# Kernel optimization log

Hardware: AMD Instinct MI355X
Metric: run time of the kernel (lower is better)

## Reference

```python
import jax, jax.numpy as jnp
import numpy as np

L, H, P = 16384, 1024, 512  # seq len, model width, state size (conj_sym: P = ssm_size//2)
DT_MIN, DT_MAX = 1e-3, 1e-1
STEP_RESCALE = 1.0


def setup_inputs() -> dict:
    key = jax.random.key(0)
    ks = jax.random.split(key, 7)
    input_sequence = jax.random.normal(ks[0], (L, H), dtype=jnp.float32)
    # Lambda: stable diagonal (Re < 0), like DPLR-HiPPO (Re = -0.5, spread imag parts)
    Lambda_re = -0.5 - jax.random.uniform(ks[1], (P,), dtype=jnp.float32)
    Lambda_im = 10.0 * jax.random.normal(ks[2], (P,), dtype=jnp.float32)
    # B (P,H,2) and C (H,P,2): real/imag stacked parameterization
    B = jax.random.normal(ks[3], (P, H, 2), dtype=jnp.float32) / np.float32(np.sqrt(H))
    C = jax.random.normal(ks[4], (H, P, 2), dtype=jnp.float32) / np.float32(np.sqrt(P))
    D = jax.random.normal(ks[5], (H,), dtype=jnp.float32)
    log_step = (jax.random.uniform(ks[6], (P, 1), dtype=jnp.float32)
                * (np.log(DT_MAX) - np.log(DT_MIN)) + np.log(DT_MIN)).astype(jnp.float32)
    return {"input_sequence": input_sequence, "Lambda_re": Lambda_re,
            "Lambda_im": Lambda_im, "B": B, "C": C, "D": D, "log_step": log_step}


def _binop(q_i, q_j):
    # diagonal linear recurrence composition; elementwise, so works on stacked arrays
    A_i, b_i = q_i
    A_j, b_j = q_j
    return (A_j * A_i, A_j * b_i + b_j)


def reference(input_sequence, Lambda_re, Lambda_im, B, C, D, log_step):
    Lambda = Lambda_re + 1j * Lambda_im                      # (P,) complex64
    B_tilde = B[..., 0] + 1j * B[..., 1]                     # (P,H)
    C_tilde = C[..., 0] + 1j * C[..., 1]                     # (H,P)
    Delta = STEP_RESCALE * jnp.exp(log_step[:, 0])           # (P,)
    # ZOH discretization
    Lambda_bar = jnp.exp(Lambda * Delta)                     # (P,)
    B_bar = ((Lambda_bar - 1.0) / Lambda)[:, None] * B_tilde # (P,H)
    # per-step scan elements
    Lambda_elements = jnp.broadcast_to(Lambda_bar, (input_sequence.shape[0], P))
    Bu_elements = jnp.einsum('lh,ph->lp', input_sequence, B_bar)  # (L,P) complex
    _, xs = jax.lax.associative_scan(_binop, (Lambda_elements, Bu_elements))
    # conj_sym readout: 2 * Re(C x)
    ys = 2.0 * jnp.einsum('lp,hp->lh', xs, C_tilde).real     # (L,H) float32
    return ys + input_sequence * D
```

## Files before the change

### kernel.cpp

```cpp
#include <hip/hip_runtime.h>
#include <math.h>

#define LL 16384
#define HH 1024
#define PP 512
#define NP2 1024
#define CHUNK 64
#define NCHUNK 256
#define BM 128
#define BN 128
#define BK 32

typedef unsigned short u16;
typedef __attribute__((ext_vector_type(8))) short bf16x8;
typedef __attribute__((ext_vector_type(4))) float f32x4;

__device__ __forceinline__ u16 f2bf(float f) {
    unsigned u = __float_as_uint(f);
    unsigned r = 0x7fffu + ((u >> 16) & 1u);
    return (u16)((u + r) >> 16);
}
__device__ __forceinline__ float bf2f(u16 x) {
    return __uint_as_float(((unsigned)x) << 16);
}

__device__ __forceinline__ void gload_lds16(const void* g, void* l) {
    __builtin_amdgcn_global_load_lds(
        (const __attribute__((address_space(1))) unsigned int*)g,
        (__attribute__((address_space(3))) unsigned int*)l, 16, 0, 0);
}

__global__ void k_setup(const float* __restrict__ lre, const float* __restrict__ lim,
                        const float* __restrict__ logstep,
                        float* __restrict__ gre, float* __restrict__ gim,
                        float* __restrict__ lbre, float* __restrict__ lbim,
                        float* __restrict__ ltre, float* __restrict__ ltim) {
    int p = threadIdx.x;
    if (p >= PP) return;
    float dt = expf(logstep[p]);
    float ar = lre[p], ai = lim[p];
    float e = expf(ar * dt);
    float s, c;
    sincosf(ai * dt, &s, &c);
    float Lr = e * c, Li = e * s;
    lbre[p] = Lr; lbim[p] = Li;
    float nr = Lr - 1.0f, ni = Li;
    float den = ar * ar + ai * ai;
    gre[p] = (nr * ar + ni * ai) / den;
    gim[p] = (ni * ar - nr * ai) / den;
    float tr = Lr, ti = Li;
    for (int i = 0; i < 6; i++) {
        float rr = tr * tr - ti * ti;
        float mm = 2.0f * tr * ti;
        tr = rr; ti = mm;
    }
    ltre[p] = tr; ltim[p] = ti;
}

__global__ void k_bbar(const float* __restrict__ B,
                       const float* __restrict__ gre, const float* __restrict__ gim,
                       u16* __restrict__ bb) {
    int t = blockIdx.x * 256 + threadIdx.x;
    int p = t >> 10;
    float2 b = ((const float2*)B)[t];
    float gr = gre[p], gi = gim[p];
    bb[t] = f2bf(gr * b.x - gi * b.y);
    bb[(size_t)PP * HH + t] = f2bf(gr * b.y + gi * b.x);
}

__global__ void k_cprep(const float* __restrict__ C, u16* __restrict__ cp) {
    int t = blockIdx.x * 256 + threadIdx.x;
    int h = t >> 9, p = t & 511;
    float2 c = ((const float2*)C)[t];
    cp[(size_t)h * NP2 + p] = f2bf(c.x);
    cp[(size_t)h * NP2 + PP + p] = f2bf(-c.y);
}

__global__ void k_cvt(const float* __restrict__ s, u16* __restrict__ d) {
    size_t i = ((size_t)blockIdx.x * 256 + threadIdx.x) * 4;
    float4 v = *(const float4*)&s[i];
    unsigned lo = (unsigned)f2bf(v.x) | ((unsigned)f2bf(v.y) << 16);
    unsigned hi = (unsigned)f2bf(v.z) | ((unsigned)f2bf(v.w) << 16);
    *(uint2*)&d[i] = make_uint2(lo, hi);
}

template<int FUSE>
__global__ __launch_bounds__(256) void k_gemm(
        const u16* __restrict__ A, const u16* __restrict__ Bt,
        void* __restrict__ outp, const int K,
        const u16* __restrict__ ubf, const float* __restrict__ Din) {
    __shared__ u16 lA[BM * BK];
    __shared__ u16 lB[BN * BK];
    const int b = blockIdx.x;
    const int xcd = b & 7, s = b >> 3;
    const int m0 = (xcd * 16 + (s >> 3)) * BM;
    const int n0 = (s & 7) * BN;
    const int N = 8 * BN;
    const int t = threadIdx.x;
    const int lane = t & 63, wid = t >> 6;
    const int wm = (wid >> 1) * 64, wn = (wid & 1) * 64;
    const int frow = lane & 15, quad = lane >> 4;

    f32x4 acc[4][4];
    #pragma unroll
    for (int i = 0; i < 4; i++)
        #pragma unroll
        for (int j = 0; j < 4; j++) acc[i][j] = (f32x4){0.f, 0.f, 0.f, 0.f};

    const int sr = t >> 2, sc = (t & 3) * 8;
    const u16* gA = A + (size_t)(m0 + sr) * K + sc;
    const u16* gB = Bt + (size_t)(n0 + sr) * K + sc;
    u16* dA = &lA[sr * BK + sc];
    u16* dB = &lB[sr * BK + sc];

    for (int k0 = 0; k0 < K; k0 += BK) {
        __syncthreads();
        gload_lds16(gA + k0, dA);
        gload_lds16(gA + (size_t)64 * K + k0, dA + 64 * BK);
        gload_lds16(gB + k0, dB);
        gload_lds16(gB + (size_t)64 * K + k0, dB + 64 * BK);
        __syncthreads();
        bf16x8 av[4], bv[4];
        #pragma unroll
        for (int i = 0; i < 4; i++)
            av[i] = *(const bf16x8*)&lA[(wm + i * 16 + frow) * BK + quad * 8];
        #pragma unroll
        for (int j = 0; j < 4; j++)
            bv[j] = *(const bf16x8*)&lB[(wn + j * 16 + frow) * BK + quad * 8];
        #pragma unroll
        for (int i = 0; i < 4; i++)
            #pragma unroll
            for (int j = 0; j < 4; j++)
                acc[i][j] = __builtin_amdgcn_mfma_f32_16x16x32_bf16(
                    av[i], bv[j], acc[i][j], 0, 0, 0);
    }

    #pragma unroll
    for (int i = 0; i < 4; i++) {
        const int row = m0 + wm + i * 16 + quad * 4;
        #pragma unroll
        for (int j = 0; j < 4; j++) {
            const int col = n0 + wn + j * 16 + frow;
            f32x4 v = acc[i][j];
            if (FUSE) {
                float* Cout = (float*)outp;
                const float dv = Din[col];
                #pragma unroll
                for (int r = 0; r < 4; r++) {
                    const size_t o = (size_t)(row + r) * N + col;
                    Cout[o] = 2.0f * v[r] + bf2f(ubf[o]) * dv;
                }
            } else {
                u16* Cb = (u16*)outp;
                #pragma unroll
                for (int r = 0; r < 4; r++)
                    Cb[(size_t)(row + r) * N + col] = f2bf(v[r]);
            }
        }
    }
}

__global__ void k_scan1(const u16* __restrict__ bu,
                        const float* __restrict__ lbre, const float* __restrict__ lbim,
                        float* __restrict__ fr, float* __restrict__ fi) {
    int p = blockIdx.x * 256 + threadIdx.x;
    int c = blockIdx.y;
    float ar = lbre[p], ai = lbim[p];
    float xr = 0.f, xi = 0.f;
    const u16* b = bu + (size_t)c * CHUNK * NP2 + p;
    for (int j = 0; j < CHUNK; j++) {
        float br = bf2f(b[0]), bi = bf2f(b[PP]);
        float nr = ar * xr - ai * xi + br;
        float ni = ar * xi + ai * xr + bi;
        xr = nr; xi = ni;
        b += NP2;
    }
    fr[c * PP + p] = xr;
    fi[c * PP + p] = xi;
}

__global__ __launch_bounds__(256) void k_scan2(
        const float* __restrict__ fr, const float* __restrict__ fi,
        const float* __restrict__ ltre, const float* __restrict__ ltim,
        float* __restrict__ cr, float* __restrict__ ci) {
    __shared__ float Ar[NCHUNK], Ai[NCHUNK], br[NCHUNK], bi[NCHUNK];
    const int p = blockIdx.x;
    const int c = threadIdx.x;
    const float lr = ltre[p], li = ltim[p];
    Ar[c] = lr; Ai[c] = li;
    br[c] = fr[c * PP + p];
    bi[c] = fi[c * PP + p];
    __syncthreads();
    #pragma unroll
    for (int d = 1; d < NCHUNK; d <<= 1) {
        float pAr = 0.f, pAi = 0.f, pbr = 0.f, pbi = 0.f;
        const bool has = (c >= d);
        if (has) { pAr = Ar[c-d]; pAi = Ai[c-d]; pbr = br[c-d]; pbi = bi[c-d]; }
        float cAr = Ar[c], cAi = Ai[c], cbr = br[c], cbi = bi[c];
        __syncthreads();
        if (has) {
            Ar[c] = cAr * pAr - cAi * pAi;
            Ai[c] = cAr * pAi + cAi * pAr;
            br[c] = cAr * pbr - cAi * pbi + cbr;
            bi[c] = cAr * pbi + cAi * pbr + cbi;
        }
        __syncthreads();
    }
    cr[c * PP + p] = (c == 0) ? 0.f : br[c-1];
    ci[c * PP + p] = (c == 0) ? 0.f : bi[c-1];
}

__global__ void k_scan3(u16* __restrict__ bu,
                        const float* __restrict__ lbre, const float* __restrict__ lbim,
                        const float* __restrict__ cr, const float* __restrict__ ci) {
    int p = blockIdx.x * 256 + threadIdx.x;
    int c = blockIdx.y;
    float ar = lbre[p], ai = lbim[p];
    float xr = cr[c * PP + p], xi = ci[c * PP + p];
    u16* b = bu + (size_t)c * CHUNK * NP2 + p;
    for (int j = 0; j < CHUNK; j++) {
        float br = bf2f(b[0]), bi = bf2f(b[PP]);
        float nr = ar * xr - ai * xi + br;
        float ni = ar * xi + ai * xr + bi;
        xr = nr; xi = ni;
        b[0] = f2bf(xr);
        b[PP] = f2bf(xi);
        b += NP2;
    }
}

extern "C" void kernel_launch(void* const* d_in, const int* in_sizes, int n_in,
                              void* d_out, int out_size, void* d_ws, size_t ws_size,
                              hipStream_t stream) {
    const float* u       = (const float*)d_in[0];
    const float* lre     = (const float*)d_in[1];
    const float* lim     = (const float*)d_in[2];
    const float* B       = (const float*)d_in[3];
    const float* C       = (const float*)d_in[4];
    const float* D       = (const float*)d_in[5];
    const float* logstep = (const float*)d_in[6];
    float* out = (float*)d_out;

    float* w = (float*)d_ws;
    float* gre  = w;
    float* gim  = w + 512;
    float* lbre = w + 1024;
    float* lbim = w + 1536;
    float* ltre = w + 2048;
    float* ltim = w + 2560;
    float* fr   = w + 4096;
    float* fi   = fr + NCHUNK * PP;
    float* cr   = fi + NCHUNK * PP;
    float* ci   = cr + NCHUNK * PP;
    u16*   bub  = (u16*)(w + (1 << 20));
    u16*   ub   = bub + (size_t)LL * NP2;
    u16*   bb   = ub + (size_t)LL * HH;
    u16*   cp   = bb + (size_t)NP2 * HH;

    k_setup<<<1, 512, 0, stream>>>(lre, lim, logstep, gre, gim, lbre, lbim, ltre, ltim);
    k_bbar<<<(PP * HH) / 256, 256, 0, stream>>>(B, gre, gim, bb);
    k_cprep<<<(HH * PP) / 256, 256, 0, stream>>>(C, cp);
    k_cvt<<<(LL * HH) / 1024, 256, 0, stream>>>(u, ub);
    k_gemm<0><<<(NP2 / BN) * (LL / BM), 256, 0, stream>>>(ub, bb, bub, HH, nullptr, nullptr);
    k_scan1<<<dim3(PP / 256, NCHUNK), 256, 0, stream>>>(bub, lbre, lbim, fr, fi);
    k_scan2<<<PP, NCHUNK, 0, stream>>>(fr, fi, ltre, ltim, cr, ci);
    k_scan3<<<dim3(PP / 256, NCHUNK), 256, 0, stream>>>(bub, lbre, lbim, cr, ci);
    k_gemm<1><<<(HH / BN) * (LL / BM), 256, 0, stream>>>(bub, cp, out, NP2, ub, D);
}
```

Before: 269.4 us.

## Swizzle GEMM LDS tiles, stage bf16 epilogue through LDS, merge prep kernels

Applies an XOR swizzle to the LDS layout of the A/B tiles in the GEMM to reduce bank conflicts on the fragment reads. For the non-fused GEMM, the bf16 output is staged through shared memory so that it is written to global memory as coalesced 16-byte stores instead of scattered 2-byte stores. The B-bar and C preparation kernels are merged into a single launch to save one kernel launch. The staged epilogue adds extra barriers and LDS traffic per output tile.

```diff
diff --git a/kernel.cpp b/kernel.cpp
--- a/kernel.cpp
+++ b/kernel.cpp
@@ -57,23 +57,24 @@
     ltre[p] = tr; ltim[p] = ti;
 }
 
-__global__ void k_bbar(const float* __restrict__ B,
-                       const float* __restrict__ gre, const float* __restrict__ gim,
-                       u16* __restrict__ bb) {
-    int t = blockIdx.x * 256 + threadIdx.x;
-    int p = t >> 10;
-    float2 b = ((const float2*)B)[t];
-    float gr = gre[p], gi = gim[p];
-    bb[t] = f2bf(gr * b.x - gi * b.y);
-    bb[(size_t)PP * HH + t] = f2bf(gr * b.y + gi * b.x);
-}
-
-__global__ void k_cprep(const float* __restrict__ C, u16* __restrict__ cp) {
-    int t = blockIdx.x * 256 + threadIdx.x;
-    int h = t >> 9, p = t & 511;
-    float2 c = ((const float2*)C)[t];
-    cp[(size_t)h * NP2 + p] = f2bf(c.x);
-    cp[(size_t)h * NP2 + PP + p] = f2bf(-c.y);
+__global__ void k_prep2(const float* __restrict__ B,
+                        const float* __restrict__ gre, const float* __restrict__ gim,
+                        const float* __restrict__ C,
+                        u16* __restrict__ bb, u16* __restrict__ cp) {
+    if (blockIdx.x < 2048) {
+        int t = blockIdx.x * 256 + threadIdx.x;
+        int p = t >> 10;
+        float2 b = ((const float2*)B)[t];
+        float gr = gre[p], gi = gim[p];
+        bb[t] = f2bf(gr * b.x - gi * b.y);
+        bb[(size_t)PP * HH + t] = f2bf(gr * b.y + gi * b.x);
+    } else {
+        int t = (blockIdx.x - 2048) * 256 + threadIdx.x;
+        int h = t >> 9, p = t & 511;
+        float2 c = ((const float2*)C)[t];
+        cp[(size_t)h * NP2 + p] = f2bf(c.x);
+        cp[(size_t)h * NP2 + PP + p] = f2bf(-c.y);
+    }
 }
 
 __global__ void k_cvt(const float* __restrict__ s, u16* __restrict__ d) {
@@ -89,8 +90,9 @@
         const u16* __restrict__ A, const u16* __restrict__ Bt,
         void* __restrict__ outp, const int K,
         const u16* __restrict__ ubf, const float* __restrict__ Din) {
-    __shared__ u16 lA[BM * BK];
-    __shared__ u16 lB[BN * BK];
+    __shared__ u16 smem[2 * BM * BK];
+    u16* lA = smem;
+    u16* lB = smem + BM * BK;
     const int b = blockIdx.x;
     const int xcd = b & 7, s = b >> 3;
     const int m0 = (xcd * 16 + (s >> 3)) * BM;
@@ -107,11 +109,12 @@
         #pragma unroll
         for (int j = 0; j < 4; j++) acc[i][j] = (f32x4){0.f, 0.f, 0.f, 0.f};
 
-    const int sr = t >> 2, sc = (t & 3) * 8;
-    const u16* gA = A + (size_t)(m0 + sr) * K + sc;
-    const u16* gB = Bt + (size_t)(n0 + sr) * K + sc;
-    u16* dA = &lA[sr * BK + sc];
-    u16* dB = &lB[sr * BK + sc];
+    const int sr = t >> 2, slot = t & 3;
+    const int seg = slot ^ ((sr >> 1) & 3);
+    const u16* gA = A + (size_t)(m0 + sr) * K + seg * 8;
+    const u16* gB = Bt + (size_t)(n0 + sr) * K + seg * 8;
+    u16* dA = &lA[sr * BK + slot * 8];
+    u16* dB = &lB[sr * BK + slot * 8];
 
     for (int k0 = 0; k0 < K; k0 += BK) {
         __syncthreads();
@@ -122,11 +125,15 @@
         __syncthreads();
         bf16x8 av[4], bv[4];
         #pragma unroll
-        for (int i = 0; i < 4; i++)
-            av[i] = *(const bf16x8*)&lA[(wm + i * 16 + frow) * BK + quad * 8];
-        #pragma unroll
-        for (int j = 0; j < 4; j++)
-            bv[j] = *(const bf16x8*)&lB[(wn + j * 16 + frow) * BK + quad * 8];
+        for (int i = 0; i < 4; i++) {
+            const int r = wm + i * 16 + frow;
+            av[i] = *(const bf16x8*)&lA[r * BK + (quad ^ ((r >> 1) & 3)) * 8];
+        }
+        #pragma unroll
+        for (int j = 0; j < 4; j++) {
+            const int r = wn + j * 16 + frow;
+            bv[j] = *(const bf16x8*)&lB[r * BK + (quad ^ ((r >> 1) & 3)) * 8];
+        }
         #pragma unroll
         for (int i = 0; i < 4; i++)
             #pragma unroll
@@ -135,27 +142,47 @@
                     av[i], bv[j], acc[i][j], 0, 0, 0);
     }
 
-    #pragma unroll
-    for (int i = 0; i < 4; i++) {
-        const int row = m0 + wm + i * 16 + quad * 4;
-        #pragma unroll
-        for (int j = 0; j < 4; j++) {
-            const int col = n0 + wn + j * 16 + frow;
-            f32x4 v = acc[i][j];
-            if (FUSE) {
-                float* Cout = (float*)outp;
+    if (FUSE) {
+        float* Cout = (float*)outp;
+        #pragma unroll
+        for (int i = 0; i < 4; i++) {
+            const int row = m0 + wm + i * 16 + quad * 4;
+            #pragma unroll
+            for (int j = 0; j < 4; j++) {
+                const int col = n0 + wn + j * 16 + frow;
                 const float dv = Din[col];
+                f32x4 v = acc[i][j];
                 #pragma unroll
                 for (int r = 0; r < 4; r++) {
                     const size_t o = (size_t)(row + r) * N + col;
                     Cout[o] = 2.0f * v[r] + bf2f(ubf[o]) * dv;
                 }
-            } else {
-                u16* Cb = (u16*)outp;
+            }
+        }
+    } else {
+        u16* Cb = (u16*)outp;
+        const int half = wm >> 6;
+        __syncthreads();
+        #pragma unroll
+        for (int i = 0; i < 4; i++) {
+            #pragma unroll
+            for (int j = 0; j < 4; j++) {
+                f32x4 v = acc[i][j];
                 #pragma unroll
                 for (int r = 0; r < 4; r++)
-                    Cb[(size_t)(row + r) * N + col] = f2bf(v[r]);
+                    smem[half * 2048 + (quad * 4 + r) * 128 + wn + j * 16 + frow]
+                        = f2bf(v[r]);
             }
+            __syncthreads();
+            #pragma unroll
+            for (int c = 0; c < 2; c++) {
+                const int fe = (t + c * 256) * 8;
+                const int hh = fe >> 11, rem = fe & 2047;
+                const int qr = rem >> 7, cb = rem & 127;
+                const int row = m0 + hh * 64 + i * 16 + qr;
+                *(uint4*)&Cb[(size_t)row * N + n0 + cb] = *(const uint4*)&smem[fe];
+            }
+            __syncthreads();
         }
     }
 }
@@ -258,8 +285,7 @@
     u16*   cp   = bb + (size_t)NP2 * HH;
 
     k_setup<<<1, 512, 0, stream>>>(lre, lim, logstep, gre, gim, lbre, lbim, ltre, ltim);
-    k_bbar<<<(PP * HH) / 256, 256, 0, stream>>>(B, gre, gim, bb);
-    k_cprep<<<(HH * PP) / 256, 256, 0, stream>>>(C, cp);
+    k_prep2<<<4096, 256, 0, stream>>>(B, gre, gim, C, bb, cp);
     k_cvt<<<(LL * HH) / 1024, 256, 0, stream>>>(u, ub);
     k_gemm<0><<<(NP2 / BN) * (LL / BM), 256, 0, stream>>>(ub, bb, bub, HH, nullptr, nullptr);
     k_scan1<<<dim3(PP / 256, NCHUNK), 256, 0, stream>>>(bub, lbre, lbim, fr, fi);
```

After: 269.0 us. No clear change (-0.1%).
